# Optimization experiments

Hardware: AMD Instinct MI355X
Metric: run time of the kernel (lower is better)

## Reference

```python
import jax, jax.numpy as jnp
import numpy as np

HEADS = 16
EPS = 1e-6

def _rmsnorm(x, g):
    # x: (..., d); norm = ||x||_2 * d^-0.5 (matches torch.norm-based RMSNorm)
    d = x.shape[-1]
    nrm = jnp.linalg.norm(x, axis=-1, keepdims=True) * (d ** -0.5)
    return x / (nrm + EPS) * g

def _rope(x, cos, sin):
    # x: (b,n,h,d) -> complex pairs over last dim; cos/sin: (1,n,1,d//2)
    b, n, h, d = x.shape
    xr = x.reshape(b, n, h, d // 2, 2)
    re, im = xr[..., 0], xr[..., 1]
    out_re = re * cos - im * sin
    out_im = re * sin + im * cos
    return jnp.stack([out_re, out_im], axis=-1).reshape(b, n, h, d)

def setup_inputs() -> dict:
    key = jax.random.key(0)
    ks = jax.random.split(key, 8)
    b, n, dim = 4, 4096, 1024
    d = dim // HEADS
    x = jax.random.normal(ks[0], (b, n, dim), dtype=jnp.float32)
    # rope freqs as cos/sin of random angles (broadcast shape 1,n,1,d//2)
    ang = jax.random.uniform(ks[1], (1, n, 1, d // 2), dtype=jnp.float32) * (2 * np.pi)
    freqs_cos = jnp.cos(ang)
    freqs_sin = jnp.sin(ang)
    sc = dim ** -0.5
    w_qkv = jax.random.normal(ks[2], (dim, 3 * dim), dtype=jnp.float32) * sc
    g_q = jnp.ones((d,), dtype=jnp.float32)
    g_k = jnp.ones((d,), dtype=jnp.float32)
    w_proj = jax.random.normal(ks[3], (dim, dim), dtype=jnp.float32) * sc
    b_proj = jnp.zeros((dim,), dtype=jnp.float32)
    return {"x": x, "freqs_cos": freqs_cos, "freqs_sin": freqs_sin,
            "w_qkv": w_qkv, "g_q": g_q, "g_k": g_k,
            "w_proj": w_proj, "b_proj": b_proj}

def reference(x, freqs_cos, freqs_sin, w_qkv, g_q, g_k, w_proj, b_proj):
    b, n, dim = x.shape
    h = HEADS
    d = dim // h
    scale = d ** -0.5
    qkv = x @ w_qkv  # (b,n,3*dim)
    q, k, v = jnp.split(qkv, 3, axis=-1)
    q = q.reshape(b, n, h, d)
    k = k.reshape(b, n, h, d)
    v = v.reshape(b, n, h, d)
    q = _rmsnorm(q, g_q)
    k = _rmsnorm(k, g_k)
    q = _rope(q, freqs_cos, freqs_sin)
    k = _rope(k, freqs_cos, freqs_sin)
    # per-token head-mixing attention: (b,n,h,h)
    attn = jnp.einsum('bnhd,bngd->bnhg', q, k) * scale
    attn = jax.nn.softmax(attn, axis=-1)
    out = jnp.einsum('bnhg,bngd->bnhd', attn, v).reshape(b, n, dim)
    return out @ w_proj + b_proj
```

## Files before the change

### kernel.cpp

```cpp
#include <hip/hip_runtime.h>
#include <hip/hip_bf16.h>
#include <stddef.h>

#define NTOK   16384
#define SEQN   4096
#define DIM    1024
#define K3     3072
#define HEADS  16
#define HD     64

typedef __attribute__((ext_vector_type(8)))  short  short8;
typedef __attribute__((ext_vector_type(16))) float  float16v;

static __device__ __forceinline__ unsigned short f32_to_bf16_bits(float f) {
    unsigned u = __float_as_uint(f);
    unsigned r = u + 0x7fffu + ((u >> 16) & 1u);
    return (unsigned short)(r >> 16);
}
static __device__ __forceinline__ unsigned pack_bf16x2(float lo, float hi) {
    return (unsigned)f32_to_bf16_bits(lo) | ((unsigned)f32_to_bf16_bits(hi) << 16);
}
static __device__ __forceinline__ void unpack_bf16x8(uint4 u, float* f) {
    f[0] = __uint_as_float(u.x << 16); f[1] = __uint_as_float(u.x & 0xffff0000u);
    f[2] = __uint_as_float(u.y << 16); f[3] = __uint_as_float(u.y & 0xffff0000u);
    f[4] = __uint_as_float(u.z << 16); f[5] = __uint_as_float(u.z & 0xffff0000u);
    f[6] = __uint_as_float(u.w << 16); f[7] = __uint_as_float(u.w & 0xffff0000u);
}

typedef const void __attribute__((address_space(1)))* gas_ptr;
typedef void __attribute__((address_space(3)))* las_ptr;
static __device__ __forceinline__ void gload_lds16(const unsigned short* g,
                                                   unsigned short* l) {
    __builtin_amdgcn_global_load_lds((gas_ptr)g, (las_ptr)l, 16, 0, 0);
}

__global__ void cvt_f32_bf16(const float4* __restrict__ in,
                             ushort4* __restrict__ out, int n4) {
    int i = blockIdx.x * blockDim.x + threadIdx.x;
    if (i < n4) {
        float4 v = in[i];
        ushort4 o;
        o.x = f32_to_bf16_bits(v.x);
        o.y = f32_to_bf16_bits(v.y);
        o.z = f32_to_bf16_bits(v.z);
        o.w = f32_to_bf16_bits(v.w);
        out[i] = o;
    }
}

__global__ void transpose_cvt(const float* __restrict__ in,
                              unsigned short* __restrict__ out,
                              int K, int N) {
    __shared__ float t[32][33];
    int n0 = blockIdx.x * 32, k0 = blockIdx.y * 32;
    int tx = threadIdx.x, ty = threadIdx.y;
    #pragma unroll
    for (int r = ty; r < 32; r += 8)
        t[r][tx] = in[(size_t)(k0 + r) * N + n0 + tx];
    __syncthreads();
    #pragma unroll
    for (int r = ty; r < 32; r += 8)
        out[(size_t)(n0 + r) * K + k0 + tx] = f32_to_bf16_bits(t[tx][r]);
}

template<int WITH_BIAS>
__global__ __launch_bounds__(256) void gemm_bf16_k64(
    const unsigned short* __restrict__ A,
    const unsigned short* __restrict__ Bt,
    void* __restrict__ Cout,
    const float* __restrict__ bias,
    int M, int N, int K)
{
    __shared__ unsigned short As[128][64];
    __shared__ unsigned short Bs[128][64];

    const int tid  = threadIdx.x;
    const int wave = tid >> 6;
    const int lane = tid & 63;
    const int l32  = lane & 31;
    const int hi   = lane >> 5;
    const int l7   = lane & 7;
    const int waveM = (wave & 1) * 64;
    const int waveN = (wave >> 1) * 64;
    const int rowBase = blockIdx.y * 128;
    const int colBase = blockIdx.x * 128;

    float16v acc[2][2];
    #pragma unroll
    for (int i = 0; i < 2; i++)
        #pragma unroll
        for (int j = 0; j < 2; j++)
            acc[i][j] = (float16v)0.0f;

    const int drow = lane >> 3;
    const int lc   = l7 ^ drow;
    const unsigned short* gA = A  + (size_t)(rowBase + wave * 32 + drow) * K + lc * 8;
    const unsigned short* gB = Bt + (size_t)(colBase + wave * 32 + drow) * K + lc * 8;
    const size_t k8 = (size_t)8 * K;

    for (int k0 = 0; k0 < K; k0 += 64) {
        __syncthreads();
        #pragma unroll
        for (int g = 0; g < 4; g++) {
            gload_lds16(gA + k0 + (size_t)g * k8, &As[wave * 32 + g * 8][0]);
            gload_lds16(gB + k0 + (size_t)g * k8, &Bs[wave * 32 + g * 8][0]);
        }
        __syncthreads();

        #pragma unroll
        for (int t = 0; t < 4; t++) {
            const int pc = ((2 * t + hi) ^ l7) * 8;
            short8 a0 = *(const short8*)&As[waveM + l32][pc];
            short8 a1 = *(const short8*)&As[waveM + 32 + l32][pc];
            short8 b0 = *(const short8*)&Bs[waveN + l32][pc];
            short8 b1 = *(const short8*)&Bs[waveN + 32 + l32][pc];
            acc[0][0] = __builtin_amdgcn_mfma_f32_32x32x16_bf16(a0, b0, acc[0][0], 0, 0, 0);
            acc[0][1] = __builtin_amdgcn_mfma_f32_32x32x16_bf16(a0, b1, acc[0][1], 0, 0, 0);
            acc[1][0] = __builtin_amdgcn_mfma_f32_32x32x16_bf16(a1, b0, acc[1][0], 0, 0, 0);
            acc[1][1] = __builtin_amdgcn_mfma_f32_32x32x16_bf16(a1, b1, acc[1][1], 0, 0, 0);
        }
    }

    #pragma unroll
    for (int i = 0; i < 2; i++) {
        #pragma unroll
        for (int j = 0; j < 2; j++) {
            const int col = colBase + waveN + j * 32 + l32;
            #pragma unroll
            for (int r = 0; r < 16; r++) {
                const int row = rowBase + waveM + i * 32
                              + (r & 3) + 8 * (r >> 2) + 4 * hi;
                float v = acc[i][j][r];
                if (WITH_BIAS) {
                    ((float*)Cout)[(size_t)row * N + col] = v + bias[col];
                } else {
                    ((unsigned short*)Cout)[(size_t)row * N + col] =
                        f32_to_bf16_bits(v);
                }
            }
        }
    }
}

__global__ __launch_bounds__(256) void attn_tok(
    const unsigned short* __restrict__ qkv,
    const float* __restrict__ fcos,
    const float* __restrict__ fsin,
    const float* __restrict__ gq,
    const float* __restrict__ gk,
    unsigned short* __restrict__ outb)
{
    __shared__ float kl[4][16][68];
    __shared__ float vl[4][16][68];

    const int tid  = threadIdx.x;
    const int wv   = tid >> 6;
    const int lane = tid & 63;
    const int h    = lane & 15;
    const int p    = lane >> 4;
    const int tok  = blockIdx.x * 4 + wv;
    const int n    = tok & (SEQN - 1);

    const unsigned short* base = qkv + (size_t)tok * K3 + h * 64 + p * 16;
    uint4 qr0 = *(const uint4*)(base);
    uint4 qr1 = *(const uint4*)(base + 8);
    uint4 kr0 = *(const uint4*)(base + DIM);
    uint4 kr1 = *(const uint4*)(base + DIM + 8);
    uint4 vr0 = *(const uint4*)(base + 2 * DIM);
    uint4 vr1 = *(const uint4*)(base + 2 * DIM + 8);

    float q[16], k[16], v[16];
    unpack_bf16x8(qr0, q); unpack_bf16x8(qr1, q + 8);
    unpack_bf16x8(kr0, k); unpack_bf16x8(kr1, k + 8);
    unpack_bf16x8(vr0, v); unpack_bf16x8(vr1, v + 8);

    float ssq = 0.f, ssk = 0.f;
    #pragma unroll
    for (int i = 0; i < 16; i++) { ssq += q[i] * q[i]; ssk += k[i] * k[i]; }
    ssq += __shfl_xor(ssq, 16); ssq += __shfl_xor(ssq, 32);
    ssk += __shfl_xor(ssk, 16); ssk += __shfl_xor(ssk, 32);
    const float sq = 1.0f / (sqrtf(ssq) * 0.125f + 1e-6f);
    const float sk = 1.0f / (sqrtf(ssk) * 0.125f + 1e-6f);

    #pragma unroll
    for (int c = 0; c < 4; c++) {
        float4 gg = *(const float4*)(gq + p * 16 + c * 4);
        float4 gh = *(const float4*)(gk + p * 16 + c * 4);
        q[c*4+0] *= sq * gg.x; q[c*4+1] *= sq * gg.y;
        q[c*4+2] *= sq * gg.z; q[c*4+3] *= sq * gg.w;
        k[c*4+0] *= sk * gh.x; k[c*4+1] *= sk * gh.y;
        k[c*4+2] *= sk * gh.z; k[c*4+3] *= sk * gh.w;
    }

    {
        const float* cb = fcos + n * 32 + p * 8;
        const float* sb = fsin + n * 32 + p * 8;
        float4 c0 = *(const float4*)cb, c1 = *(const float4*)(cb + 4);
        float4 s0 = *(const float4*)sb, s1 = *(const float4*)(sb + 4);
        float cs[8] = {c0.x,c0.y,c0.z,c0.w,c1.x,c1.y,c1.z,c1.w};
        float sn[8] = {s0.x,s0.y,s0.z,s0.w,s1.x,s1.y,s1.z,s1.w};
        #pragma unroll
        for (int j = 0; j < 8; j++) {
            float re = q[2*j], im = q[2*j+1];
            q[2*j]   = re * cs[j] - im * sn[j];
            q[2*j+1] = re * sn[j] + im * cs[j];
            re = k[2*j]; im = k[2*j+1];
            k[2*j]   = re * cs[j] - im * sn[j];
            k[2*j+1] = re * sn[j] + im * cs[j];
        }
    }

    {
        float* krow = &kl[wv][h][p * 16];
        float* vrow = &vl[wv][h][p * 16];
        #pragma unroll
        for (int c = 0; c < 4; c++) {
            *(float4*)(krow + c*4) = make_float4(k[c*4], k[c*4+1], k[c*4+2], k[c*4+3]);
            *(float4*)(vrow + c*4) = make_float4(v[c*4], v[c*4+1], v[c*4+2], v[c*4+3]);
        }
    }

    float s[16];
    #pragma unroll
    for (int g = 0; g < 16; g++) {
        const float* kg = &kl[wv][g][p * 16];
        float4 a0 = *(const float4*)(kg);
        float4 a1 = *(const float4*)(kg + 4);
        float4 a2 = *(const float4*)(kg + 8);
        float4 a3 = *(const float4*)(kg + 12);
        s[g] = q[0]*a0.x + q[1]*a0.y + q[2]*a0.z + q[3]*a0.w
             + q[4]*a1.x + q[5]*a1.y + q[6]*a1.z + q[7]*a1.w
             + q[8]*a2.x + q[9]*a2.y + q[10]*a2.z + q[11]*a2.w
             + q[12]*a3.x + q[13]*a3.y + q[14]*a3.z + q[15]*a3.w;
    }
    #pragma unroll
    for (int g = 0; g < 16; g++) {
        s[g] += __shfl_xor(s[g], 16);
        s[g] += __shfl_xor(s[g], 32);
        s[g] *= 0.125f;
    }

    float m = s[0];
    #pragma unroll
    for (int g = 1; g < 16; g++) m = fmaxf(m, s[g]);
    float sum = 0.f;
    #pragma unroll
    for (int g = 0; g < 16; g++) { s[g] = __expf(s[g] - m); sum += s[g]; }
    const float inv = 1.0f / sum;

    float o[16];
    #pragma unroll
    for (int i = 0; i < 16; i++) o[i] = 0.f;
    #pragma unroll
    for (int g = 0; g < 16; g++) {
        const float pg = s[g] * inv;
        const float* vg = &vl[wv][g][p * 16];
        float4 b0 = *(const float4*)(vg);
        float4 b1 = *(const float4*)(vg + 4);
        float4 b2 = *(const float4*)(vg + 8);
        float4 b3 = *(const float4*)(vg + 12);
        o[0]  += pg * b0.x; o[1]  += pg * b0.y; o[2]  += pg * b0.z; o[3]  += pg * b0.w;
        o[4]  += pg * b1.x; o[5]  += pg * b1.y; o[6]  += pg * b1.z; o[7]  += pg * b1.w;
        o[8]  += pg * b2.x; o[9]  += pg * b2.y; o[10] += pg * b2.z; o[11] += pg * b2.w;
        o[12] += pg * b3.x; o[13] += pg * b3.y; o[14] += pg * b3.z; o[15] += pg * b3.w;
    }

    uint4 r0, r1;
    r0.x = pack_bf16x2(o[0],  o[1]);  r0.y = pack_bf16x2(o[2],  o[3]);
    r0.z = pack_bf16x2(o[4],  o[5]);  r0.w = pack_bf16x2(o[6],  o[7]);
    r1.x = pack_bf16x2(o[8],  o[9]);  r1.y = pack_bf16x2(o[10], o[11]);
    r1.z = pack_bf16x2(o[12], o[13]); r1.w = pack_bf16x2(o[14], o[15]);
    unsigned short* ob = outb + (size_t)tok * DIM + h * 64 + p * 16;
    *(uint4*)(ob)     = r0;
    *(uint4*)(ob + 8) = r1;
}

extern "C" void kernel_launch(void* const* d_in, const int* in_sizes, int n_in,
                              void* d_out, int out_size, void* d_ws, size_t ws_size,
                              hipStream_t stream) {
    const float* x      = (const float*)d_in[0];
    const float* fcos   = (const float*)d_in[1];
    const float* fsin   = (const float*)d_in[2];
    const float* w_qkv  = (const float*)d_in[3];
    const float* g_q    = (const float*)d_in[4];
    const float* g_k    = (const float*)d_in[5];
    const float* w_proj = (const float*)d_in[6];
    const float* b_proj = (const float*)d_in[7];
    float* out = (float*)d_out;

    char* ws = (char*)d_ws;
    unsigned short* xb      = (unsigned short*)(ws);
    unsigned short* wqkvT   = (unsigned short*)(ws + 33554432);
    unsigned short* wprojT  = (unsigned short*)(ws + 39845888);
    unsigned short* qkv     = (unsigned short*)(ws + 41943040);
    unsigned short* attnout = (unsigned short*)(ws + 142606336);
    (void)ws_size; (void)in_sizes; (void)n_in; (void)out_size;

    {
        int n4 = (NTOK * DIM) / 4;
        cvt_f32_bf16<<<(n4 + 255) / 256, 256, 0, stream>>>(
            (const float4*)x, (ushort4*)xb, n4);
        transpose_cvt<<<dim3(K3 / 32, DIM / 32), dim3(32, 8), 0, stream>>>(
            w_qkv, wqkvT, DIM, K3);
        transpose_cvt<<<dim3(DIM / 32, DIM / 32), dim3(32, 8), 0, stream>>>(
            w_proj, wprojT, DIM, DIM);
    }
    gemm_bf16_k64<0><<<dim3(K3 / 128, NTOK / 128), 256, 0, stream>>>(
        xb, wqkvT, (void*)qkv, nullptr, NTOK, K3, DIM);
    attn_tok<<<NTOK / 4, 256, 0, stream>>>(qkv, fcos, fsin, g_q, g_k, attnout);
    gemm_bf16_k64<1><<<dim3(DIM / 128, NTOK / 128), 256, 0, stream>>>(
        attnout, wprojT, (void*)out, b_proj, NTOK, DIM, DIM);
}
```

Measured before the change: 365.3 us.

## Rewrite GEMM as 256x256 double-buffered, wave-specialized pipelined MFMA kernel

Replaces the 128x128 single-buffered GEMM with a 256x256-tile, 512-thread kernel. It double-buffers LDS, interleaves global-to-LDS prefetch with 16x16x32 MFMA compute in a hand-scheduled loop using explicit waitcnt, barriers and setprio, and swizzles block order for L2 locality. The goal is to hide memory latency and raise arithmetic intensity for both projection GEMMs. K is now hardcoded to 1024, and the larger tiles and LDS footprint may reduce occupancy and produce few blocks for the N=1024 projection.

```diff
diff --git a/kernel.cpp b/kernel.cpp
--- a/kernel.cpp
+++ b/kernel.cpp
@@ -10,7 +10,7 @@
 #define HD     64
 
 typedef __attribute__((ext_vector_type(8)))  short  short8;
-typedef __attribute__((ext_vector_type(16))) float  float16v;
+typedef __attribute__((ext_vector_type(4)))  float  float4v;
 
 static __device__ __forceinline__ unsigned short f32_to_bf16_bits(float f) {
     unsigned u = __float_as_uint(f);
@@ -64,82 +64,163 @@
 }
 
 template<int WITH_BIAS>
-__global__ __launch_bounds__(256) void gemm_bf16_k64(
+__global__ __launch_bounds__(512, 2) void gemm_bf16_256(
     const unsigned short* __restrict__ A,
     const unsigned short* __restrict__ Bt,
     void* __restrict__ Cout,
     const float* __restrict__ bias,
-    int M, int N, int K)
+    int M, int N)
 {
-    __shared__ unsigned short As[128][64];
-    __shared__ unsigned short Bs[128][64];
+    constexpr int K = 1024;
+    __shared__ unsigned short As[2][256][64];
+    __shared__ unsigned short Bs[2][256][64];
 
     const int tid  = threadIdx.x;
     const int wave = tid >> 6;
     const int lane = tid & 63;
-    const int l32  = lane & 31;
-    const int hi   = lane >> 5;
+    const int wm   = wave >> 2;
+    const int wn   = wave & 3;
+    const int l15  = lane & 15;
+    const int l4   = lane >> 4;
     const int l7   = lane & 7;
-    const int waveM = (wave & 1) * 64;
-    const int waveN = (wave >> 1) * 64;
-    const int rowBase = blockIdx.y * 128;
-    const int colBase = blockIdx.x * 128;
-
-    float16v acc[2][2];
-    #pragma unroll
-    for (int i = 0; i < 2; i++)
-        #pragma unroll
-        for (int j = 0; j < 2; j++)
-            acc[i][j] = (float16v)0.0f;
+
+    const int nwg = (int)gridDim.x;
+    const int bid = (int)blockIdx.x;
+    const int swz = (bid & 7) * (nwg >> 3) + (bid >> 3);
+    const int ntn = N >> 8;
+    const int rowBase = (swz / ntn) << 8;
+    const int colBase = (swz % ntn) << 8;
+    (void)M;
 
     const int drow = lane >> 3;
     const int lc   = l7 ^ drow;
-    const unsigned short* gA = A  + (size_t)(rowBase + wave * 32 + drow) * K + lc * 8;
-    const unsigned short* gB = Bt + (size_t)(colBase + wave * 32 + drow) * K + lc * 8;
-    const size_t k8 = (size_t)8 * K;
-
-    for (int k0 = 0; k0 < K; k0 += 64) {
-        __syncthreads();
+    const unsigned short* gA = A  + (size_t)(rowBase + drow) * K + lc * 8;
+    const unsigned short* gB = Bt + (size_t)(colBase + drow) * K + lc * 8;
+
+    float4v acc[8][4];
+    #pragma unroll
+    for (int m = 0; m < 8; m++)
         #pragma unroll
-        for (int g = 0; g < 4; g++) {
-            gload_lds16(gA + k0 + (size_t)g * k8, &As[wave * 32 + g * 8][0]);
-            gload_lds16(gB + k0 + (size_t)g * k8, &Bs[wave * 32 + g * 8][0]);
-        }
-        __syncthreads();
-
+        for (int n = 0; n < 4; n++) acc[m][n] = (float4v)0.0f;
+
+    short8 aF[4][2], b0F[2][2], b1F[2][2];
+
+#define STG_A(f, oddH, T) do {                                               \
+    const int ra_ = ((wave >> 2) * 128) + (oddH) * 64 + (wave & 3) * 16;     \
+    gload_lds16(gA + (size_t)(ra_    ) * K + (size_t)(T) * 64, &As[f][ra_    ][0]); \
+    gload_lds16(gA + (size_t)(ra_ + 8) * K + (size_t)(T) * 64, &As[f][ra_ + 8][0]); \
+  } while (0)
+#define STG_B(f, oddH, T) do {                                               \
+    const int rb_ = ((wave >> 1) * 64) + (oddH) * 32 + (wave & 1) * 16;      \
+    gload_lds16(gB + (size_t)(rb_    ) * K + (size_t)(T) * 64, &Bs[f][rb_    ][0]); \
+    gload_lds16(gB + (size_t)(rb_ + 8) * K + (size_t)(T) * 64, &Bs[f][rb_ + 8][0]); \
+  } while (0)
+
+#define RD_A(f, a) do {                                                      \
+    _Pragma("unroll")                                                        \
+    for (int ra = 0; ra < 4; ra++) {                                         \
+      const unsigned short* r_ = &As[f][wm * 128 + (a) * 64 + ra * 16 + l15][0]; \
+      aF[ra][0] = *(const short8*)(r_ + (((    l4) ^ l7) * 8));              \
+      aF[ra][1] = *(const short8*)(r_ + (((4 + l4) ^ l7) * 8));              \
+    } } while (0)
+#define RD_B(f, b, dst) do {                                                 \
+    _Pragma("unroll")                                                        \
+    for (int cb = 0; cb < 2; cb++) {                                         \
+      const unsigned short* r_ = &Bs[f][wn * 64 + (b) * 32 + cb * 16 + l15][0]; \
+      dst[cb][0] = *(const short8*)(r_ + (((    l4) ^ l7) * 8));             \
+      dst[cb][1] = *(const short8*)(r_ + (((4 + l4) ^ l7) * 8));             \
+    } } while (0)
+
+#define MM(a, b, bF) do {                                                    \
+    _Pragma("unroll")                                                        \
+    for (int ra = 0; ra < 4; ra++)                                           \
+      _Pragma("unroll")                                                      \
+      for (int cb = 0; cb < 2; cb++) {                                       \
+        acc[(a)*4+ra][(b)*2+cb] = __builtin_amdgcn_mfma_f32_16x16x32_bf16(   \
+            aF[ra][0], bF[cb][0], acc[(a)*4+ra][(b)*2+cb], 0, 0, 0);         \
+        acc[(a)*4+ra][(b)*2+cb] = __builtin_amdgcn_mfma_f32_16x16x32_bf16(   \
+            aF[ra][1], bF[cb][1], acc[(a)*4+ra][(b)*2+cb], 0, 0, 0);         \
+      } } while (0)
+
+#define BAR()   do { __builtin_amdgcn_s_barrier(); \
+                     __builtin_amdgcn_sched_barrier(0); } while (0)
+#define LGKM0() do { asm volatile("s_waitcnt lgkmcnt(0)" ::: "memory"); \
+                     __builtin_amdgcn_sched_barrier(0); } while (0)
+#define VM(n)   do { asm volatile("s_waitcnt vmcnt(" #n ")" ::: "memory"); \
+                     __builtin_amdgcn_sched_barrier(0); } while (0)
+#define P1()    __builtin_amdgcn_s_setprio(1)
+#define P0()    __builtin_amdgcn_s_setprio(0)
+
+    STG_A(0,0,0); STG_B(0,0,0); STG_B(0,1,0); STG_A(0,1,0);
+    STG_A(1,0,1); STG_B(1,0,1); STG_B(1,1,1);
+    VM(6);
+    BAR();
+
+    #pragma unroll 1
+    for (int i = 0; i < 7; i++) {
+        const int t1 = 2 * i + 1;
+        RD_A(0,0); RD_B(0,0,b0F); STG_A(1,1,t1);
+        BAR(); LGKM0(); P1(); MM(0,0,b0F); P0(); BAR();
+        RD_B(0,1,b1F);            STG_A(0,0,t1+1);
+        BAR(); LGKM0(); P1(); MM(0,1,b1F); P0(); BAR();
+        RD_A(0,1);                STG_B(0,0,t1+1);
+        BAR(); LGKM0(); P1(); MM(1,1,b1F); P0(); BAR();
+                                  STG_B(0,1,t1+1); VM(6);
+        BAR(); LGKM0(); P1(); MM(1,0,b0F); P0(); BAR();
+        RD_A(1,0); RD_B(1,0,b0F); STG_A(0,1,t1+1);
+        BAR(); LGKM0(); P1(); MM(0,0,b0F); P0(); BAR();
+        RD_B(1,1,b1F);            STG_A(1,0,t1+2);
+        BAR(); LGKM0(); P1(); MM(0,1,b1F); P0(); BAR();
+        RD_A(1,1);                STG_B(1,0,t1+2);
+        BAR(); LGKM0(); P1(); MM(1,1,b1F); P0(); BAR();
+                                  STG_B(1,1,t1+2); VM(6);
+        BAR(); LGKM0(); P1(); MM(1,0,b0F); P0(); BAR();
+    }
+
+    {
+        RD_A(0,0); RD_B(0,0,b0F); STG_A(1,1,15);
+        BAR(); LGKM0(); P1(); MM(0,0,b0F); P0(); BAR();
+        RD_B(0,1,b1F);
+        BAR(); LGKM0(); P1(); MM(0,1,b1F); P0(); BAR();
+        RD_A(0,1);
+        BAR(); LGKM0(); P1(); MM(1,1,b1F); P0(); BAR();
+        VM(0);
+        BAR(); LGKM0(); P1(); MM(1,0,b0F); P0(); BAR();
+        RD_A(1,0); RD_B(1,0,b0F); LGKM0(); P1(); MM(0,0,b0F); P0();
+        RD_B(1,1,b1F);            LGKM0(); P1(); MM(0,1,b1F); P0();
+        RD_A(1,1);                LGKM0(); P1(); MM(1,1,b1F); P0();
+                                           P1(); MM(1,0,b0F); P0();
+    }
+
+    #pragma unroll
+    for (int m = 0; m < 8; m++) {
+        const int row = rowBase + wm * 128 + m * 16 + l4 * 4;
         #pragma unroll
-        for (int t = 0; t < 4; t++) {
-            const int pc = ((2 * t + hi) ^ l7) * 8;
-            short8 a0 = *(const short8*)&As[waveM + l32][pc];
-            short8 a1 = *(const short8*)&As[waveM + 32 + l32][pc];
-            short8 b0 = *(const short8*)&Bs[waveN + l32][pc];
-            short8 b1 = *(const short8*)&Bs[waveN + 32 + l32][pc];
-            acc[0][0] = __builtin_amdgcn_mfma_f32_32x32x16_bf16(a0, b0, acc[0][0], 0, 0, 0);
-            acc[0][1] = __builtin_amdgcn_mfma_f32_32x32x16_bf16(a0, b1, acc[0][1], 0, 0, 0);
-            acc[1][0] = __builtin_amdgcn_mfma_f32_32x32x16_bf16(a1, b0, acc[1][0], 0, 0, 0);
-            acc[1][1] = __builtin_amdgcn_mfma_f32_32x32x16_bf16(a1, b1, acc[1][1], 0, 0, 0);
-        }
-    }
-
-    #pragma unroll
-    for (int i = 0; i < 2; i++) {
-        #pragma unroll
-        for (int j = 0; j < 2; j++) {
-            const int col = colBase + waveN + j * 32 + l32;
-            #pragma unroll
-            for (int r = 0; r < 16; r++) {
-                const int row = rowBase + waveM + i * 32
-                              + (r & 3) + 8 * (r >> 2) + 4 * hi;
-                float v = acc[i][j][r];
-                if (WITH_BIAS) {
-                    ((float*)Cout)[(size_t)row * N + col] = v + bias[col];
-                } else {
-                    ((unsigned short*)Cout)[(size_t)row * N + col] =
-                        f32_to_bf16_bits(v);
-                }
+        for (int n = 0; n < 4; n++) {
+            const int col = colBase + wn * 64 + n * 16 + l15;
+            if (WITH_BIAS) {
+                const float bv = bias[col];
+                #pragma unroll
+                for (int r = 0; r < 4; r++)
+                    ((float*)Cout)[(size_t)(row + r) * N + col] = acc[m][n][r] + bv;
+            } else {
+                #pragma unroll
+                for (int r = 0; r < 4; r++)
+                    ((unsigned short*)Cout)[(size_t)(row + r) * N + col] =
+                        f32_to_bf16_bits(acc[m][n][r]);
             }
         }
     }
+#undef STG_A
+#undef STG_B
+#undef RD_A
+#undef RD_B
+#undef MM
+#undef BAR
+#undef LGKM0
+#undef VM
+#undef P1
+#undef P0
 }
 
 __global__ __launch_bounds__(256) void attn_tok(
@@ -305,9 +386,9 @@
         transpose_cvt<<<dim3(DIM / 32, DIM / 32), dim3(32, 8), 0, stream>>>(
             w_proj, wprojT, DIM, DIM);
     }
-    gemm_bf16_k64<0><<<dim3(K3 / 128, NTOK / 128), 256, 0, stream>>>(
-        xb, wqkvT, (void*)qkv, nullptr, NTOK, K3, DIM);
+    gemm_bf16_256<0><<<dim3((NTOK / 256) * (K3 / 256)), 512, 0, stream>>>(
+        xb, wqkvT, (void*)qkv, nullptr, NTOK, K3);
     attn_tok<<<NTOK / 4, 256, 0, stream>>>(qkv, fcos, fsin, g_q, g_k, attnout);
-    gemm_bf16_k64<1><<<dim3(DIM / 128, NTOK / 128), 256, 0, stream>>>(
-        attnout, wprojT, (void*)out, b_proj, NTOK, DIM, DIM);
-}
+    gemm_bf16_256<1><<<dim3((NTOK / 256) * (DIM / 256)), 512, 0, stream>>>(
+        attnout, wprojT, (void*)out, b_proj, NTOK, DIM);
+}
```

New measurement: 332.4 us. 1.1x faster.
